# Performance work log

Hardware: AMD Instinct MI355X
Metric: run time of the kernel (lower is better)

Reference implementation:

```python
import jax, jax.numpy as jnp
import numpy as np

B, H, W, C = 32, 256, 256, 4
KH, KW, F = 5, 5, 8


def setup_inputs() -> dict:
    key = jax.random.key(0)
    kx, kk = jax.random.split(key)
    x = jax.random.normal(kx, (B, H, W, C), dtype=jnp.float32)
    kernel = jax.random.normal(kk, (KH, KW, C, F), dtype=jnp.float32) * 0.1
    return {"x": x, "kernel": kernel}


def reference(x, kernel):
    """Multi-filter grayscale erosion (min-plus correlation), channels-last.

    out[b, y, x, f] = min_{dy, dx, c} ( x[b, y+dy, x+dx, c] - kernel[dy, dx, c, f] )
    (stride 1, VALID padding, rates 1 -- matching tf.nn.erosion2d followed by
    a min-reduction over the input-channel axis, per output filter.)
    """
    kh, kw, c, f = kernel.shape
    b, h, w, _ = x.shape
    ho, wo = h - kh + 1, w - kw + 1  # VALID output size
    out = None
    # Fixed, small structural loop over the kh*kw window taps; each tap is a
    # fully vectorized shifted slice + min-plus reduction over channels.
    for i in range(kh):
        for j in range(kw):
            patch = x[:, i:i + ho, j:j + wo, :]                      # [B,Ho,Wo,C]
            # min over channels of (patch - kernel tap): [B,Ho,Wo,F]
            v = jnp.min(patch[..., :, None] - kernel[i, j][None, None, None, :, :], axis=3)
            out = v if out is None else jnp.minimum(out, v)
    return out
```

## Files before the change

kernel.cpp:

```cpp
#include <hip/hip_runtime.h>

#define BB 32
#define HH 256
#define WW 256
#define CC 4
#define KH 5
#define KW 5
#define FF 8
#define HO (HH - KH + 1)
#define WO (WW - KW + 1)
#define PX 2
#define WOP (WO / PX)

typedef _Float16 h2     __attribute__((ext_vector_type(2)));
typedef __fp16   fp16x2 __attribute__((ext_vector_type(2)));

static __device__ __forceinline__ h2 pkrtz(float a, float b) {
    fp16x2 r = __builtin_amdgcn_cvt_pkrtz(a, b);
    return __builtin_bit_cast(h2, r);
}

__global__ void pack_kernel(const float* __restrict__ k, unsigned int* __restrict__ kp)
{
    int i = blockIdx.x * blockDim.x + threadIdx.x;
    if (i >= KH * KW * FF * 2) return;
    int t = i >> 4;
    int r = i & 15;
    int f = r >> 1;
    int p = r & 1;
    float a = k[(t * CC + 2 * p + 0) * FF + f];
    float b = k[(t * CC + 2 * p + 1) * FF + f];
    kp[i] = __builtin_bit_cast(unsigned int, pkrtz(a, b));
}

__global__ __launch_bounds__(256) void erosion2d_f16(
    const float* __restrict__ x,
    const h2* __restrict__ k2,
    float* __restrict__ out)
{
    const int total = BB * HO * WOP;
    int tid = blockIdx.x * blockDim.x + threadIdx.x;
    if (tid >= total) return;

    int b   = tid / (HO * WOP);
    int rem = tid - b * (HO * WOP);
    int y   = rem / WOP;
    int xo  = (rem - y * WOP) * PX;

    const float* xb = x + (((size_t)b * HH + y) * WW + xo) * CC;

    h2 acc[PX][FF];
    const h2 big = { (_Float16)65504.0f, (_Float16)65504.0f };
#pragma unroll
    for (int p = 0; p < PX; ++p)
#pragma unroll
        for (int f = 0; f < FF; ++f)
            acc[p][f] = big;

#pragma unroll
    for (int dy = 0; dy < KH; ++dy) {
#pragma unroll
        for (int dxx = 0; dxx < KW + PX - 1; ++dxx) {
            const float4 px = *reinterpret_cast<const float4*>(xb + (dy * WW + dxx) * CC);
            const h2 p01 = pkrtz(px.x, px.y);
            const h2 p23 = pkrtz(px.z, px.w);
#pragma unroll
            for (int p = 0; p < PX; ++p) {
                const int dx = dxx - p;
                if (dx < 0 || dx >= KW) continue;
                const h2* kt = k2 + ((dy * KW + dx) * FF) * 2;
#pragma unroll
                for (int f = 0; f < FF; ++f) {
                    h2 d01 = p01 - kt[f * 2 + 0];
                    h2 d23 = p23 - kt[f * 2 + 1];
                    acc[p][f] = __builtin_elementwise_min(
                        acc[p][f], __builtin_elementwise_min(d01, d23));
                }
            }
        }
    }

#pragma unroll
    for (int p = 0; p < PX; ++p) {
        float r[FF];
#pragma unroll
        for (int f = 0; f < FF; ++f)
            r[f] = fminf((float)acc[p][f][0], (float)acc[p][f][1]);
        float* op = out + ((size_t)tid * PX + p) * FF;
        *reinterpret_cast<float4*>(op)     = make_float4(r[0], r[1], r[2], r[3]);
        *reinterpret_cast<float4*>(op + 4) = make_float4(r[4], r[5], r[6], r[7]);
    }
}

extern "C" void kernel_launch(void* const* d_in, const int* in_sizes, int n_in,
                              void* d_out, int out_size, void* d_ws, size_t ws_size,
                              hipStream_t stream) {
    const float* x = (const float*)d_in[0];
    const float* k = (const float*)d_in[1];
    float* out = (float*)d_out;

    pack_kernel<<<2, 256, 0, stream>>>(k, (unsigned int*)d_ws);

    const int total = BB * HO * WOP;
    const int block = 256;
    const int grid  = (total + block - 1) / block;
    erosion2d_f16<<<grid, block, 0, stream>>>(x, (const h2*)d_ws, out);
}
```

Baseline: 64.53 us.

## Tile 2x2 outputs per thread and pack fp16 pairs along filters

Each thread now computes a 2x2 block of output pixels instead of 1x2, so every loaded input row is reused across two output rows. The kernel is repacked so each fp16 pair holds two filters for one channel, with the input value broadcast into both lanes. This removes the final lane-combining min and keeps the same number of packed min/sub ops per tap. The aim is to cut redundant global loads and f32-to-f16 conversions, at the cost of more registers and half as many threads.

```diff
diff --git a/kernel.cpp b/kernel.cpp
--- a/kernel.cpp
+++ b/kernel.cpp
@@ -10,7 +10,11 @@
 #define HO (HH - KH + 1)
 #define WO (WW - KW + 1)
 #define PX 2
-#define WOP (WO / PX)
+#define PY 2
+#define NXT (WO / PX)
+#define NYT (HO / PY)
+#define NROW (PY + KH - 1)
+#define NCOL (PX + KW - 1)
 
 typedef _Float16 h2     __attribute__((ext_vector_type(2)));
 typedef __fp16   fp16x2 __attribute__((ext_vector_type(2)));
@@ -23,13 +27,12 @@
 __global__ void pack_kernel(const float* __restrict__ k, unsigned int* __restrict__ kp)
 {
     int i = blockIdx.x * blockDim.x + threadIdx.x;
-    if (i >= KH * KW * FF * 2) return;
-    int t = i >> 4;
-    int r = i & 15;
-    int f = r >> 1;
-    int p = r & 1;
-    float a = k[(t * CC + 2 * p + 0) * FF + f];
-    float b = k[(t * CC + 2 * p + 1) * FF + f];
+    if (i >= KH * KW * CC * FF / 2) return;
+    int tap = i >> 4;
+    int c   = (i >> 2) & 3;
+    int fp  = i & 3;
+    float a = k[(tap * CC + c) * FF + 2 * fp + 0];
+    float b = k[(tap * CC + c) * FF + 2 * fp + 1];
     kp[i] = __builtin_bit_cast(unsigned int, pkrtz(a, b));
 }
 
@@ -38,57 +41,76 @@
     const h2* __restrict__ k2,
     float* __restrict__ out)
 {
-    const int total = BB * HO * WOP;
+    const int total = BB * NYT * NXT;
     int tid = blockIdx.x * blockDim.x + threadIdx.x;
     if (tid >= total) return;
 
-    int b   = tid / (HO * WOP);
-    int rem = tid - b * (HO * WOP);
-    int y   = rem / WOP;
-    int xo  = (rem - y * WOP) * PX;
+    int b   = tid / (NYT * NXT);
+    int rem = tid - b * (NYT * NXT);
+    int yt  = rem / NXT;
+    int xt  = rem - yt * NXT;
+    const int y0 = yt * PY;
+    const int x0 = xt * PX;
 
-    const float* xb = x + (((size_t)b * HH + y) * WW + xo) * CC;
+    const float* xb = x + (((size_t)b * HH + y0) * WW + x0) * CC;
 
-    h2 acc[PX][FF];
+    h2 acc[PY][PX][FF / 2];
     const h2 big = { (_Float16)65504.0f, (_Float16)65504.0f };
 #pragma unroll
-    for (int p = 0; p < PX; ++p)
+    for (int py = 0; py < PY; ++py)
 #pragma unroll
-        for (int f = 0; f < FF; ++f)
-            acc[p][f] = big;
+        for (int p = 0; p < PX; ++p)
+#pragma unroll
+            for (int fp = 0; fp < FF / 2; ++fp)
+                acc[py][p][fp] = big;
 
 #pragma unroll
-    for (int dy = 0; dy < KH; ++dy) {
+    for (int r = 0; r < NROW; ++r) {
+        h2 xbc[NCOL][CC];
 #pragma unroll
-        for (int dxx = 0; dxx < KW + PX - 1; ++dxx) {
-            const float4 px = *reinterpret_cast<const float4*>(xb + (dy * WW + dxx) * CC);
-            const h2 p01 = pkrtz(px.x, px.y);
-            const h2 p23 = pkrtz(px.z, px.w);
+        for (int j = 0; j < NCOL; ++j) {
+            const float4 px = *reinterpret_cast<const float4*>(xb + (r * WW + j) * CC);
+            xbc[j][0] = pkrtz(px.x, px.x);
+            xbc[j][1] = pkrtz(px.y, px.y);
+            xbc[j][2] = pkrtz(px.z, px.z);
+            xbc[j][3] = pkrtz(px.w, px.w);
+        }
 #pragma unroll
-            for (int p = 0; p < PX; ++p) {
-                const int dx = dxx - p;
-                if (dx < 0 || dx >= KW) continue;
-                const h2* kt = k2 + ((dy * KW + dx) * FF) * 2;
+        for (int py = 0; py < PY; ++py) {
+            const int dy = r - py;
+            if (dy < 0 || dy >= KH) continue;
 #pragma unroll
-                for (int f = 0; f < FF; ++f) {
-                    h2 d01 = p01 - kt[f * 2 + 0];
-                    h2 d23 = p23 - kt[f * 2 + 1];
-                    acc[p][f] = __builtin_elementwise_min(
-                        acc[p][f], __builtin_elementwise_min(d01, d23));
+            for (int dx = 0; dx < KW; ++dx) {
+                const h2* kt = k2 + (dy * KW + dx) * (CC * FF / 2);
+#pragma unroll
+                for (int p = 0; p < PX; ++p) {
+#pragma unroll
+                    for (int c = 0; c < CC; ++c) {
+                        const h2 xv = xbc[dx + p][c];
+#pragma unroll
+                        for (int fp = 0; fp < FF / 2; ++fp) {
+                            h2 d = xv - kt[c * (FF / 2) + fp];
+                            acc[py][p][fp] =
+                                __builtin_elementwise_min(acc[py][p][fp], d);
+                        }
+                    }
                 }
             }
         }
     }
 
 #pragma unroll
-    for (int p = 0; p < PX; ++p) {
-        float r[FF];
+    for (int py = 0; py < PY; ++py) {
 #pragma unroll
-        for (int f = 0; f < FF; ++f)
-            r[f] = fminf((float)acc[p][f][0], (float)acc[p][f][1]);
-        float* op = out + ((size_t)tid * PX + p) * FF;
-        *reinterpret_cast<float4*>(op)     = make_float4(r[0], r[1], r[2], r[3]);
-        *reinterpret_cast<float4*>(op + 4) = make_float4(r[4], r[5], r[6], r[7]);
+        for (int p = 0; p < PX; ++p) {
+            float* op = out + (((size_t)b * HO + (y0 + py)) * WO + (x0 + p)) * FF;
+            float4 o0 = make_float4((float)acc[py][p][0][0], (float)acc[py][p][0][1],
+                                    (float)acc[py][p][1][0], (float)acc[py][p][1][1]);
+            float4 o1 = make_float4((float)acc[py][p][2][0], (float)acc[py][p][2][1],
+                                    (float)acc[py][p][3][0], (float)acc[py][p][3][1]);
+            *reinterpret_cast<float4*>(op)     = o0;
+            *reinterpret_cast<float4*>(op + 4) = o1;
+        }
     }
 }
 
@@ -101,7 +123,7 @@
 
     pack_kernel<<<2, 256, 0, stream>>>(k, (unsigned int*)d_ws);
 
-    const int total = BB * HO * WOP;
+    const int total = BB * NYT * NXT;
     const int block = 256;
     const int grid  = (total + block - 1) / block;
     erosion2d_f16<<<grid, block, 0, stream>>>(x, (const h2*)d_ws, out);
```

Measured after the change: 74.24 us. 15.0% more time.
